# Optimization experiments

Hardware: AMD Instinct MI355X
Metric: run time of the kernel (lower is better)

## Reference

```python
import jax, jax.numpy as jnp
import numpy as np

N_USERS = 150000
N_ENTITIES = 250000
CH = 64
N_REL = 17
N_FACTORS = 4
N_EDGES = 1_000_000
NNZ = 1_000_000
N_HOPS = 2


def setup_inputs() -> dict:
    key = jax.random.key(0)
    ks = jax.random.split(key, 10)
    user_emb = jax.random.normal(ks[0], (N_USERS, CH), jnp.float32) * 0.1
    entity_emb = jax.random.normal(ks[1], (N_ENTITIES, CH), jnp.float32) * 0.1
    latent_emb = jax.random.normal(ks[2], (N_FACTORS, CH), jnp.float32) * 0.1
    weight = jax.random.normal(ks[3], (N_REL - 1, CH), jnp.float32) * 0.1
    disen_weight_att = jax.random.normal(ks[4], (N_FACTORS, N_REL - 1), jnp.float32) * 0.1
    edge_index = jax.random.randint(ks[5], (2, N_EDGES), 0, N_ENTITIES)
    edge_type = jax.random.randint(ks[6], (N_EDGES,), 1, N_REL)  # in [1, N_REL-1]
    inter_row = jax.random.randint(ks[7], (NNZ,), 0, N_USERS)
    inter_col = jax.random.randint(ks[8], (NNZ,), 0, N_ENTITIES)
    inter_val = jax.random.uniform(ks[9], (NNZ,), jnp.float32)
    return {
        "user_emb": user_emb, "entity_emb": entity_emb, "latent_emb": latent_emb,
        "weight": weight, "disen_weight_att": disen_weight_att, "inter_val": inter_val,
        "edge_index": edge_index, "edge_type": edge_type,
        "inter_row": inter_row, "inter_col": inter_col,
    }


def _l2norm(x):
    # F.normalize(x, dim=1) with eps=1e-12
    n = jnp.linalg.norm(x, axis=1, keepdims=True)
    return x / jnp.maximum(n, 1e-12)


def reference(user_emb, entity_emb, latent_emb, weight, disen_weight_att,
              inter_val, edge_index, edge_type, inter_row, inter_col):
    n_entities = entity_emb.shape[0]
    n_users = user_emb.shape[0]
    head, tail = edge_index[0], edge_index[1]

    # _cul_cor with ind='cosine': sum_{i<j} cos(w_i, w_j)^2 over rows of disen_weight_att
    wn = disen_weight_att / jnp.linalg.norm(disen_weight_att, axis=1, keepdims=True)
    gram = (wn @ wn.T) ** 2  # [F, F]
    cor = jnp.sum(jnp.triu(gram, k=1))

    # constants across hops
    counts = jax.ops.segment_sum(jnp.ones(head.shape[0], jnp.float32), head,
                                 num_segments=n_entities)
    denom = jnp.maximum(counts, 1.0)[:, None]  # scatter_mean denominator (0 -> keep 0)
    disen_weight = jax.nn.softmax(disen_weight_att, axis=-1) @ weight  # [F, C]

    e, u = entity_emb, user_emb
    ent_res, usr_res = entity_emb, user_emb
    for _ in range(N_HOPS):
        # KG aggregate: per-edge gather, relation modulation, scatter_mean into heads
        neigh = e[tail] * weight[edge_type - 1]              # [E, C]
        entity_agg = jax.ops.segment_sum(neigh, head, num_segments=n_entities) / denom

        # user -> latent factor attention
        score = jax.nn.softmax(u @ latent_emb.T, axis=1)[:, :, None]  # [U, F, 1]

        # user aggregate: sparse interact_mat @ entity_emb
        user_agg = jax.ops.segment_sum(inter_val[:, None] * e[inter_col], inter_row,
                                       num_segments=n_users)  # [U, C]
        mix = jnp.sum(disen_weight[None, :, :] * score, axis=1)  # [U, C]
        user_agg = user_agg * mix + user_agg

        e = _l2norm(entity_agg)
        u = _l2norm(user_agg)
        ent_res = ent_res + e
        usr_res = usr_res + u
    return ent_res, usr_res, cor
```

## Files before the change

### kernel.cpp

```cpp
#include <hip/hip_runtime.h>
#include <hip/hip_bf16.h>

#define N_USERS    150000
#define N_ENTITIES 250000
#define CHN        64
#define N_RELM1    16
#define N_FACTORS  4
#define N_EDGES    1000000
#define NNZ_       1000000
#define NRECS      (N_EDGES + NNZ_)

#define BROWS      1024
#define RCAP       8192
#define RCAP_OUT   8192
#define EBUCKETS   245
#define USR0       (EBUCKETS * BROWS)
#define ROWS_EFF   (USR0 + N_USERS)
#define NB         392
#define TILE_A     4096
#define TA_THREADS 512
#define ITEMS_A    8
#define BIN_BLOCKS 489
#define CONV_N4    (N_ENTITIES * CHN / 4)
#define CONV_BLOCKS ((CONV_N4 + 511) / 512)

typedef float vf4 __attribute__((ext_vector_type(4)));

__device__ __forceinline__ unsigned short f2bf(float f) {
    unsigned u = __float_as_uint(f);
    return (unsigned short)((u + 0x7fffu + ((u >> 16) & 1u)) >> 16);
}

__global__ __launch_bounds__(512) void build_kernel(
    const int* __restrict__ head, const int* __restrict__ tail,
    const int* __restrict__ etype, const int* __restrict__ irow,
    const int* __restrict__ icol, const float* __restrict__ val,
    int* __restrict__ bcur, unsigned long long* __restrict__ binned,
    const float* __restrict__ weight, const float* __restrict__ att,
    float* __restrict__ disenw, float* __restrict__ cor_out,
    const float4* __restrict__ esrc, ushort4* __restrict__ ebf0)
{
    int blk = blockIdx.x;
    int tid = threadIdx.x;

    if (blk < BIN_BLOCKS) {
        __shared__ int cntS[NB], startS[NB], gbase[NB];
        __shared__ unsigned long long buf[TILE_A];
        __shared__ unsigned short bk[TILE_A];

        if (tid < NB) cntS[tid] = 0;
        __syncthreads();

        int base = blk * TILE_A;
        unsigned long long p[ITEMS_A];
        int bkt[ITEMS_A], rnk[ITEMS_A];
        #pragma unroll
        for (int j = 0; j < ITEMS_A; ++j) {
            int i = base + j * TA_THREADS + tid;
            bkt[j] = -1;
            if (i < NRECS) {
                int row; unsigned long long pay;
                if (i < N_EDGES) {
                    row = head[i];
                    pay = ((unsigned long long)(unsigned)(etype[i] - 1) << 18) | (unsigned)tail[i];
                } else {
                    int jj = i - N_EDGES;
                    row = USR0 + irow[jj];
                    pay = ((unsigned long long)__float_as_uint(val[jj]) << 18) | (unsigned)icol[jj];
                }
                p[j] = pay | ((unsigned long long)(unsigned)(row & (BROWS - 1)) << 50);
                bkt[j] = row >> 10;
                rnk[j] = atomicAdd(&cntS[bkt[j]], 1);
            }
        }
        __syncthreads();
        if (tid == 0) {
            int s = 0;
            for (int b = 0; b < NB; ++b) { startS[b] = s; s += cntS[b]; }
        }
        __syncthreads();
        if (tid < NB && cntS[tid] > 0)
            gbase[tid] = tid * RCAP + atomicAdd(&bcur[tid], cntS[tid]);
        __syncthreads();

        #pragma unroll
        for (int j = 0; j < ITEMS_A; ++j) {
            if (bkt[j] >= 0) {
                int s = startS[bkt[j]] + rnk[j];
                buf[s] = p[j];
                bk[s] = (unsigned short)bkt[j];
            }
        }
        __syncthreads();

        int total = startS[NB - 1] + cntS[NB - 1];
        for (int s = tid; s < total; s += TA_THREADS) {
            int b = bk[s];
            int dst = gbase[b] + (s - startS[b]);
            if (dst < (b + 1) * RCAP) binned[dst] = buf[s];
        }
    } else if (blk == BIN_BLOCKS) {
        if (tid < 256) {
            int f  = tid >> 6;
            int ch = tid & 63;
            float m = -1e30f;
            for (int r = 0; r < N_RELM1; ++r) m = fmaxf(m, att[f * N_RELM1 + r]);
            float ex[N_RELM1];
            float s = 0.f;
            for (int r = 0; r < N_RELM1; ++r) { ex[r] = expf(att[f * N_RELM1 + r] - m); s += ex[r]; }
            float inv = 1.f / s;
            float acc = 0.f;
            for (int r = 0; r < N_RELM1; ++r) acc += (ex[r] * inv) * weight[r * CHN + ch];
            disenw[f * CHN + ch] = acc;
        }
        if (tid == 0) {
            float wn[N_FACTORS][N_RELM1];
            for (int i = 0; i < N_FACTORS; ++i) {
                float ss = 0.f;
                for (int r = 0; r < N_RELM1; ++r) { float v = att[i * N_RELM1 + r]; ss += v * v; }
                float innv = 1.f / sqrtf(ss);
                for (int r = 0; r < N_RELM1; ++r) wn[i][r] = att[i * N_RELM1 + r] * innv;
            }
            float cor = 0.f;
            for (int i = 0; i < N_FACTORS; ++i)
                for (int j = i + 1; j < N_FACTORS; ++j) {
                    float d = 0.f;
                    for (int r = 0; r < N_RELM1; ++r) d += wn[i][r] * wn[j][r];
                    cor += d * d;
                }
            cor_out[0] = cor;
        }
    } else {
        int i = (blk - BIN_BLOCKS - 1) * 512 + tid;
        if (i < CONV_N4) {
            float4 v = esrc[i];
            ebf0[i] = make_ushort4(f2bf(v.x), f2bf(v.y), f2bf(v.z), f2bf(v.w));
        }
    }
}

__global__ __launch_bounds__(512) void bucket_scatter_kernel(
    const unsigned long long* __restrict__ binned,
    const int* __restrict__ bcur,
    unsigned int* __restrict__ recsE,
    unsigned long long* __restrict__ recsU,
    uint4* __restrict__ headerE,
    uint4* __restrict__ headerU)
{
    __shared__ int rowcnt[BROWS];
    __shared__ int sExcl[BROWS];
    __shared__ int sA[512], sB[512];
    __shared__ unsigned int hdr0[BROWS], hdr1[BROWS], hdr2[BROWS];

    int tid = threadIdx.x;
    int b = blockIdx.x;
    rowcnt[2 * tid] = 0;
    rowcnt[2 * tid + 1] = 0;
    hdr0[2 * tid] = 0; hdr0[2 * tid + 1] = 0;
    hdr1[2 * tid] = 0; hdr1[2 * tid + 1] = 0;
    hdr2[2 * tid] = 0; hdr2[2 * tid + 1] = 0;
    __syncthreads();

    int s0 = b * RCAP;
    int nrec = bcur[b];
    if (nrec > RCAP) nrec = RCAP;
    int s1 = s0 + nrec;

    for (int i = s0 + tid; i < s1; i += 512) {
        int rowlo = (int)(binned[i] >> 50) & (BROWS - 1);
        atomicAdd(&rowcnt[rowlo], 1);
    }
    __syncthreads();

    int c0 = rowcnt[2 * tid];
    int c1 = rowcnt[2 * tid + 1];
    int pc0 = (c0 + 1) & ~1;
    int pc1 = (c1 + 1) & ~1;
    sA[tid] = pc0 + pc1;
    __syncthreads();
    int* src = sA; int* dst = sB;
    #pragma unroll
    for (int off = 1; off < 512; off <<= 1) {
        dst[tid] = src[tid] + ((tid >= off) ? src[tid - off] : 0);
        __syncthreads();
        int* tm = src; src = dst; dst = tm;
    }
    int excl = src[tid] - (pc0 + pc1);

    int gbaseOut = (b < EBUCKETS ? b : b - EBUCKETS) * RCAP_OUT;
    __syncthreads();
    rowcnt[2 * tid] = excl;
    rowcnt[2 * tid + 1] = excl + pc0;
    sExcl[2 * tid] = excl;
    sExcl[2 * tid + 1] = excl + pc0;
    __syncthreads();

    if (b < EBUCKETS) {
        for (int i = s0 + tid; i < s1; i += 512) {
            unsigned long long p = binned[i];
            int rowlo = (int)(p >> 50) & (BROWS - 1);
            int local = atomicAdd(&rowcnt[rowlo], 1);
            unsigned rec = (unsigned)(p & ((1ull << 50) - 1));
            recsE[gbaseOut + local] = rec;
            int rank = local - sExcl[rowlo];
            if (rank == 0) hdr0[rowlo] = rec;
            else if (rank == 1) hdr1[rowlo] = rec;
            else if (rank == 2) hdr2[rowlo] = rec;
        }
        __syncthreads();
        int grow = b * BROWS;
        #pragma unroll
        for (int t = 0; t < 2; ++t) {
            int r = 2 * tid + t;
            int row = grow + r;
            if (row < N_ENTITIES) {
                unsigned co = ((unsigned)((t == 0) ? c0 : c1) << 22) |
                              (unsigned)(gbaseOut + sExcl[r]);
                headerE[row] = make_uint4(co, hdr0[r], hdr1[r], hdr2[r]);
            }
        }
    } else {
        for (int i = s0 + tid; i < s1; i += 512) {
            unsigned long long p = binned[i];
            int rowlo = (int)(p >> 50) & (BROWS - 1);
            int local = atomicAdd(&rowcnt[rowlo], 1);
            unsigned long long rec = p & ((1ull << 50) - 1);
            recsU[gbaseOut + local] = rec;
            int rank = local - sExcl[rowlo];
            if (rank == 0) { hdr0[rowlo] = (unsigned)rec; hdr1[rowlo] = (unsigned)(rec >> 32); }
        }
        __syncthreads();
        int grow = b * BROWS - USR0;
        #pragma unroll
        for (int t = 0; t < 2; ++t) {
            int r = 2 * tid + t;
            int urow = grow + r;
            if (urow >= 0 && urow < N_USERS) {
                unsigned co = ((unsigned)((t == 0) ? c0 : c1) << 22) |
                              (unsigned)(gbaseOut + sExcl[r]);
                headerU[urow] = make_uint4(co, hdr0[r], hdr1[r], 0u);
            }
        }
    }
}

__device__ __forceinline__ void fma8w(uint4 g, const float* __restrict__ w, float* acc) {
    acc[0] += __uint_as_float(g.x << 16)          * w[0];
    acc[1] += __uint_as_float(g.x & 0xffff0000u)  * w[1];
    acc[2] += __uint_as_float(g.y << 16)          * w[2];
    acc[3] += __uint_as_float(g.y & 0xffff0000u)  * w[3];
    acc[4] += __uint_as_float(g.z << 16)          * w[4];
    acc[5] += __uint_as_float(g.z & 0xffff0000u)  * w[5];
    acc[6] += __uint_as_float(g.w << 16)          * w[6];
    acc[7] += __uint_as_float(g.w & 0xffff0000u)  * w[7];
}
__device__ __forceinline__ void fma8v(uint4 g, float v, float* acc) {
    acc[0] += __uint_as_float(g.x << 16)          * v;
    acc[1] += __uint_as_float(g.x & 0xffff0000u)  * v;
    acc[2] += __uint_as_float(g.y << 16)          * v;
    acc[3] += __uint_as_float(g.y & 0xffff0000u)  * v;
    acc[4] += __uint_as_float(g.z << 16)          * v;
    acc[5] += __uint_as_float(g.z & 0xffff0000u)  * v;
    acc[6] += __uint_as_float(g.w << 16)          * v;
    acc[7] += __uint_as_float(g.w & 0xffff0000u)  * v;
}
__device__ __forceinline__ void bf8_unpack(uint4 g, float* o) {
    o[0] = __uint_as_float(g.x << 16); o[1] = __uint_as_float(g.x & 0xffff0000u);
    o[2] = __uint_as_float(g.y << 16); o[3] = __uint_as_float(g.y & 0xffff0000u);
    o[4] = __uint_as_float(g.z << 16); o[5] = __uint_as_float(g.z & 0xffff0000u);
    o[6] = __uint_as_float(g.w << 16); o[7] = __uint_as_float(g.w & 0xffff0000u);
}

template<int PASS>
__global__ __launch_bounds__(256) void hop_kernel(
    const unsigned short* __restrict__ ebf,
    const unsigned int* __restrict__ recsE,
    const unsigned long long* __restrict__ recsU,
    const uint4* __restrict__ headerE,
    const uint4* __restrict__ headerU,
    const float* __restrict__ weight,
    const float* __restrict__ latent,
    const float* __restrict__ disenw,
    const float* __restrict__ u_emb,
    const float* __restrict__ e_emb,
    const unsigned short* __restrict__ ubfA,
    unsigned short* __restrict__ ebf_new,
    unsigned short* __restrict__ ubf_new,
    float* __restrict__ out_ent,
    float* __restrict__ out_usr)
{
    __shared__ float wl[N_RELM1 * CHN];
    for (int k = threadIdx.x; k < N_RELM1 * CHN; k += 256) wl[k] = weight[k];
    __syncthreads();

    unsigned idx = blockIdx.x * 256u + threadIdx.x;
    unsigned row = idx >> 3;
    int sub = idx & 7;
    int chb = sub * 8;

    float acc[8] = {0.f,0.f,0.f,0.f,0.f,0.f,0.f,0.f};

    if (row < N_ENTITIES) {
        uint4 h = headerE[row];
        int n = h.x >> 22;
        int start = h.x & 0x3FFFFF;
        if (n > 0) {
            uint4 g = *(const uint4*)(ebf + (size_t)(h.y & 0x3FFFF) * CHN + chb);
            fma8w(g, &wl[(h.y >> 18) * CHN + chb], acc);
        }
        if (n > 1) {
            uint4 g = *(const uint4*)(ebf + (size_t)(h.z & 0x3FFFF) * CHN + chb);
            fma8w(g, &wl[(h.z >> 18) * CHN + chb], acc);
        }
        if (n > 2) {
            uint4 g = *(const uint4*)(ebf + (size_t)(h.w & 0x3FFFF) * CHN + chb);
            fma8w(g, &wl[(h.w >> 18) * CHN + chb], acc);
        }
        int k = 3;
        for (; k + 4 <= n; k += 4) {
            unsigned r0 = recsE[start + k];
            unsigned r1 = recsE[start + k + 1];
            unsigned r2 = recsE[start + k + 2];
            unsigned r3 = recsE[start + k + 3];
            uint4 g0 = *(const uint4*)(ebf + (size_t)(r0 & 0x3FFFF) * CHN + chb);
            uint4 g1 = *(const uint4*)(ebf + (size_t)(r1 & 0x3FFFF) * CHN + chb);
            uint4 g2 = *(const uint4*)(ebf + (size_t)(r2 & 0x3FFFF) * CHN + chb);
            uint4 g3 = *(const uint4*)(ebf + (size_t)(r3 & 0x3FFFF) * CHN + chb);
            fma8w(g0, &wl[(r0 >> 18) * CHN + chb], acc);
            fma8w(g1, &wl[(r1 >> 18) * CHN + chb], acc);
            fma8w(g2, &wl[(r2 >> 18) * CHN + chb], acc);
            fma8w(g3, &wl[(r3 >> 18) * CHN + chb], acc);
        }
        for (; k < n; ++k) {
            unsigned r0 = recsE[start + k];
            uint4 g0 = *(const uint4*)(ebf + (size_t)(r0 & 0x3FFFF) * CHN + chb);
            fma8w(g0, &wl[(r0 >> 18) * CHN + chb], acc);
        }
        float inv_d = (n > 0) ? (1.f / (float)n) : 1.f;
        float ss = 0.f;
        #pragma unroll
        for (int i = 0; i < 8; ++i) { acc[i] *= inv_d; ss += acc[i] * acc[i]; }
        ss += __shfl_xor(ss, 1, 64);
        ss += __shfl_xor(ss, 2, 64);
        ss += __shfl_xor(ss, 4, 64);
        float innv = 1.f / fmaxf(sqrtf(ss), 1e-12f);
        float y[8];
        #pragma unroll
        for (int i = 0; i < 8; ++i) y[i] = acc[i] * innv;
        if (PASS == 1) {
            uint4 pk;
            pk.x = (unsigned)f2bf(y[0]) | ((unsigned)f2bf(y[1]) << 16);
            pk.y = (unsigned)f2bf(y[2]) | ((unsigned)f2bf(y[3]) << 16);
            pk.z = (unsigned)f2bf(y[4]) | ((unsigned)f2bf(y[5]) << 16);
            pk.w = (unsigned)f2bf(y[6]) | ((unsigned)f2bf(y[7]) << 16);
            *(uint4*)(ebf_new + (size_t)row * CHN + chb) = pk;
        } else {
            float y1[8];
            bf8_unpack(*(const uint4*)(ebf + (size_t)row * CHN + chb), y1);
            const vf4* bp = (const vf4*)&e_emb[(size_t)row * CHN + chb];
            vf4 b0 = __builtin_nontemporal_load(bp);
            vf4 b1 = __builtin_nontemporal_load(bp + 1);
            vf4* op = (vf4*)&out_ent[(size_t)row * CHN + chb];
            vf4 o0 = {b0.x + y1[0] + y[0], b0.y + y1[1] + y[1], b0.z + y1[2] + y[2], b0.w + y1[3] + y[3]};
            vf4 o1 = {b1.x + y1[4] + y[4], b1.y + y1[5] + y[5], b1.z + y1[6] + y[6], b1.w + y1[7] + y[7]};
            __builtin_nontemporal_store(o0, op);
            __builtin_nontemporal_store(o1, op + 1);
        }
    } else if (row >= USR0 && row < ROWS_EFF) {
        unsigned ur = row - USR0;
        uint4 h = headerU[ur];
        int n = h.x >> 22;
        int start = h.x & 0x3FFFFF;

        if (n > 0) {
            unsigned long long q = ((unsigned long long)h.z << 32) | h.y;
            uint4 g = *(const uint4*)(ebf + (size_t)(q & 0x3FFFFu) * CHN + chb);
            fma8v(g, __uint_as_float((unsigned)(q >> 18)), acc);
        }
        int k = 1;
        for (; k + 4 <= n; k += 4) {
            unsigned long long q0 = recsU[start + k];
            unsigned long long q1 = recsU[start + k + 1];
            unsigned long long q2 = recsU[start + k + 2];
            unsigned long long q3 = recsU[start + k + 3];
            uint4 g0 = *(const uint4*)(ebf + (size_t)(q0 & 0x3FFFFu) * CHN + chb);
            uint4 g1 = *(const uint4*)(ebf + (size_t)(q1 & 0x3FFFFu) * CHN + chb);
            uint4 g2 = *(const uint4*)(ebf + (size_t)(q2 & 0x3FFFFu) * CHN + chb);
            uint4 g3 = *(const uint4*)(ebf + (size_t)(q3 & 0x3FFFFu) * CHN + chb);
            fma8v(g0, __uint_as_float((unsigned)(q0 >> 18)), acc);
            fma8v(g1, __uint_as_float((unsigned)(q1 >> 18)), acc);
            fma8v(g2, __uint_as_float((unsigned)(q2 >> 18)), acc);
            fma8v(g3, __uint_as_float((unsigned)(q3 >> 18)), acc);
        }
        for (; k < n; ++k) {
            unsigned long long q0 = recsU[start + k];
            uint4 g0 = *(const uint4*)(ebf + (size_t)(q0 & 0x3FFFFu) * CHN + chb);
            fma8v(g0, __uint_as_float((unsigned)(q0 >> 18)), acc);
        }

        float uo[8];
        if (PASS == 1) {
            const float4* up = (const float4*)&u_emb[(size_t)ur * CHN + chb];
            float4 a0 = up[0], a1 = up[1];
            uo[0]=a0.x; uo[1]=a0.y; uo[2]=a0.z; uo[3]=a0.w;
            uo[4]=a1.x; uo[5]=a1.y; uo[6]=a1.z; uo[7]=a1.w;
        } else {
            bf8_unpack(*(const uint4*)(ubfA + (size_t)ur * CHN + chb), uo);
        }

        float dotv[N_FACTORS];
        #pragma unroll
        for (int f = 0; f < N_FACTORS; ++f) {
            const float4* lp = (const float4*)&latent[f * CHN + chb];
            float4 l0 = lp[0], l1 = lp[1];
            float p = uo[0] * l0.x + uo[1] * l0.y + uo[2] * l0.z + uo[3] * l0.w
                    + uo[4] * l1.x + uo[5] * l1.y + uo[6] * l1.z + uo[7] * l1.w;
            p += __shfl_xor(p, 1, 64);
            p += __shfl_xor(p, 2, 64);
            p += __shfl_xor(p, 4, 64);
            dotv[f] = p;
        }
        float m = fmaxf(fmaxf(dotv[0], dotv[1]), fmaxf(dotv[2], dotv[3]));
        float es = 0.f;
        #pragma unroll
        for (int f = 0; f < N_FACTORS; ++f) { dotv[f] = expf(dotv[f] - m); es += dotv[f]; }
        float sinv = 1.f / es;
        float mix[8] = {0.f,0.f,0.f,0.f,0.f,0.f,0.f,0.f};
        #pragma unroll
        for (int f = 0; f < N_FACTORS; ++f) {
            float sc = dotv[f] * sinv;
            const float4* dp = (const float4*)&disenw[f * CHN + chb];
            float4 d0 = dp[0], d1 = dp[1];
            mix[0] += sc * d0.x; mix[1] += sc * d0.y; mix[2] += sc * d0.z; mix[3] += sc * d0.w;
            mix[4] += sc * d1.x; mix[5] += sc * d1.y; mix[6] += sc * d1.z; mix[7] += sc * d1.w;
        }

        float ss = 0.f;
        #pragma unroll
        for (int i = 0; i < 8; ++i) { acc[i] *= (1.f + mix[i]); ss += acc[i] * acc[i]; }
        ss += __shfl_xor(ss, 1, 64);
        ss += __shfl_xor(ss, 2, 64);
        ss += __shfl_xor(ss, 4, 64);
        float innv = 1.f / fmaxf(sqrtf(ss), 1e-12f);
        float y[8];
        #pragma unroll
        for (int i = 0; i < 8; ++i) y[i] = acc[i] * innv;
        if (PASS == 1) {
            uint4 pk;
            pk.x = (unsigned)f2bf(y[0]) | ((unsigned)f2bf(y[1]) << 16);
            pk.y = (unsigned)f2bf(y[2]) | ((unsigned)f2bf(y[3]) << 16);
            pk.z = (unsigned)f2bf(y[4]) | ((unsigned)f2bf(y[5]) << 16);
            pk.w = (unsigned)f2bf(y[6]) | ((unsigned)f2bf(y[7]) << 16);
            *(uint4*)(ubf_new + (size_t)ur * CHN + chb) = pk;
        } else {
            const vf4* bp = (const vf4*)&u_emb[(size_t)ur * CHN + chb];
            vf4 b0 = __builtin_nontemporal_load(bp);
            vf4 b1 = __builtin_nontemporal_load(bp + 1);
            vf4* op = (vf4*)&out_usr[(size_t)ur * CHN + chb];
            vf4 o0 = {b0.x + uo[0] + y[0], b0.y + uo[1] + y[1], b0.z + uo[2] + y[2], b0.w + uo[3] + y[3]};
            vf4 o1 = {b1.x + uo[4] + y[4], b1.y + uo[5] + y[5], b1.z + uo[6] + y[6], b1.w + uo[7] + y[7]};
            __builtin_nontemporal_store(o0, op);
            __builtin_nontemporal_store(o1, op + 1);
        }
    }
}

extern "C" void kernel_launch(void* const* d_in, const int* in_sizes, int n_in,
                              void* d_out, int out_size, void* d_ws, size_t ws_size,
                              hipStream_t stream) {
    const float* user_emb   = (const float*)d_in[0];
    const float* entity_emb = (const float*)d_in[1];
    const float* latent_emb = (const float*)d_in[2];
    const float* weight     = (const float*)d_in[3];
    const float* att        = (const float*)d_in[4];
    const float* inter_val  = (const float*)d_in[5];
    const int*   edge_index = (const int*)d_in[6];
    const int*   edge_type  = (const int*)d_in[7];
    const int*   inter_row  = (const int*)d_in[8];
    const int*   inter_col  = (const int*)d_in[9];

    const int* head = edge_index;
    const int* tail = edge_index + N_EDGES;

    float* out_ent = (float*)d_out;
    float* out_usr = out_ent + (size_t)N_ENTITIES * CHN;
    float* out_cor = out_usr + (size_t)N_USERS * CHN;

    char* ws = (char*)d_ws;
    unsigned short* ebf0   = (unsigned short*)ws;
    unsigned short* ebfA   = (unsigned short*)(ws + 32000000);
    unsigned short* ubfA   = (unsigned short*)(ws + 64000000);
    unsigned long long* binned = (unsigned long long*)(ws + 83200000);
    unsigned long long* recsU  = (unsigned long long*)(ws + 108890112);
    unsigned int* recsE    = (unsigned int*)(ws + 118523904);
    float* disenw          = (float*)(ws + 126552064);
    uint4* headerE         = (uint4*)(ws + 126553088);
    uint4* headerU         = (uint4*)(ws + 130553088);
    int*   bcur            = (int*)(ws + 132953088);

    hipMemsetAsync(bcur, 0, NB * sizeof(int), stream);

    build_kernel<<<BIN_BLOCKS + 1 + CONV_BLOCKS, 512, 0, stream>>>(
        head, tail, edge_type, inter_row, inter_col, inter_val,
        bcur, binned, weight, att, disenw, out_cor,
        (const float4*)entity_emb, (ushort4*)ebf0);

    bucket_scatter_kernel<<<NB, 512, 0, stream>>>(binned, bcur, recsE, recsU,
                                                  headerE, headerU);

    const int hop_blocks = (ROWS_EFF * 8 + 255) / 256;

    hop_kernel<1><<<hop_blocks, 256, 0, stream>>>(ebf0, recsE, recsU, headerE, headerU,
                                                  weight, latent_emb, disenw,
                                                  user_emb, entity_emb, nullptr,
                                                  ebfA, ubfA, nullptr, nullptr);

    hop_kernel<2><<<hop_blocks, 256, 0, stream>>>(ebfA, recsE, recsU, headerE, headerU,
                                                  weight, latent_emb, disenw,
                                                  user_emb, entity_emb, ubfA,
                                                  nullptr, nullptr, out_ent, out_usr);
}
```

Measured before the change: 223.5 us.

## Sort rows by degree within buckets to balance hop kernel wavefronts

The bucket scatter kernel now builds a per-bucket permutation of rows grouped by their edge count (capped at 63) using a shared-memory histogram. The hop kernels read this permutation so that rows of similar degree land in the same wavefront, which cuts divergence from uneven per-row loop lengths. In exchange, every hop thread does one extra indirect load and row writes lose their sequential order within a bucket. Slots for padding rows are marked invalid and skipped.

Measured after the change: 235.4 us. 1.05x slower.

```diff
diff --git a/kernel.cpp b/kernel.cpp
--- a/kernel.cpp
+++ b/kernel.cpp
@@ -17,6 +17,7 @@
 #define USR0       (EBUCKETS * BROWS)
 #define ROWS_EFF   (USR0 + N_USERS)
 #define NB         392
+#define NSLOTS     (NB * BROWS)
 #define TILE_A     4096
 #define TA_THREADS 512
 #define ITEMS_A    8
@@ -145,12 +146,14 @@
     unsigned int* __restrict__ recsE,
     unsigned long long* __restrict__ recsU,
     uint4* __restrict__ headerE,
-    uint4* __restrict__ headerU)
+    uint4* __restrict__ headerU,
+    unsigned int* __restrict__ perm)
 {
     __shared__ int rowcnt[BROWS];
     __shared__ int sExcl[BROWS];
     __shared__ int sA[512], sB[512];
     __shared__ unsigned int hdr0[BROWS], hdr1[BROWS], hdr2[BROWS];
+    __shared__ int dh[64], dhoff[64];
 
     int tid = threadIdx.x;
     int b = blockIdx.x;
@@ -159,6 +162,7 @@
     hdr0[2 * tid] = 0; hdr0[2 * tid + 1] = 0;
     hdr1[2 * tid] = 0; hdr1[2 * tid + 1] = 0;
     hdr2[2 * tid] = 0; hdr2[2 * tid + 1] = 0;
+    if (tid < 64) dh[tid] = 0;
     __syncthreads();
 
     int s0 = b * RCAP;
@@ -193,6 +197,24 @@
     rowcnt[2 * tid + 1] = excl + pc0;
     sExcl[2 * tid] = excl;
     sExcl[2 * tid + 1] = excl + pc0;
+
+    int grow = b * BROWS;
+    bool v0, v1;
+    if (b < EBUCKETS) { v0 = (grow + 2 * tid) < N_ENTITIES; v1 = (grow + 2 * tid + 1) < N_ENTITIES; }
+    else              { v0 = (grow + 2 * tid) < ROWS_EFF;   v1 = (grow + 2 * tid + 1) < ROWS_EFF; }
+    int key0 = v0 ? min(c0, 63) : 0;
+    int key1 = v1 ? min(c1, 63) : 0;
+    int rank0 = atomicAdd(&dh[key0], 1);
+    int rank1 = atomicAdd(&dh[key1], 1);
+    __syncthreads();
+    if (tid == 0) {
+        int s = 0;
+        #pragma unroll
+        for (int i = 0; i < 64; ++i) { dhoff[i] = s; s += dh[i]; }
+    }
+    __syncthreads();
+    perm[grow + dhoff[key0] + rank0] = v0 ? (unsigned)(grow + 2 * tid)     : 0xFFFFFFFFu;
+    perm[grow + dhoff[key1] + rank1] = v1 ? (unsigned)(grow + 2 * tid + 1) : 0xFFFFFFFFu;
     __syncthreads();
 
     if (b < EBUCKETS) {
@@ -208,7 +230,6 @@
             else if (rank == 2) hdr2[rowlo] = rec;
         }
         __syncthreads();
-        int grow = b * BROWS;
         #pragma unroll
         for (int t = 0; t < 2; ++t) {
             int r = 2 * tid + t;
@@ -230,11 +251,11 @@
             if (rank == 0) { hdr0[rowlo] = (unsigned)rec; hdr1[rowlo] = (unsigned)(rec >> 32); }
         }
         __syncthreads();
-        int grow = b * BROWS - USR0;
+        int ubase = grow - USR0;
         #pragma unroll
         for (int t = 0; t < 2; ++t) {
             int r = 2 * tid + t;
-            int urow = grow + r;
+            int urow = ubase + r;
             if (urow >= 0 && urow < N_USERS) {
                 unsigned co = ((unsigned)((t == 0) ? c0 : c1) << 22) |
                               (unsigned)(gbaseOut + sExcl[r]);
@@ -278,6 +299,7 @@
     const unsigned long long* __restrict__ recsU,
     const uint4* __restrict__ headerE,
     const uint4* __restrict__ headerU,
+    const unsigned int* __restrict__ perm,
     const float* __restrict__ weight,
     const float* __restrict__ latent,
     const float* __restrict__ disenw,
@@ -294,9 +316,11 @@
     __syncthreads();
 
     unsigned idx = blockIdx.x * 256u + threadIdx.x;
-    unsigned row = idx >> 3;
+    unsigned slot = idx >> 3;
     int sub = idx & 7;
     int chb = sub * 8;
+    if (slot >= NSLOTS) return;
+    unsigned row = perm[slot];
 
     float acc[8] = {0.f,0.f,0.f,0.f,0.f,0.f,0.f,0.f};
 
@@ -366,7 +390,7 @@
             __builtin_nontemporal_store(o0, op);
             __builtin_nontemporal_store(o1, op + 1);
         }
-    } else if (row >= USR0 && row < ROWS_EFF) {
+    } else if (row < ROWS_EFF) {
         unsigned ur = row - USR0;
         uint4 h = headerU[ur];
         int n = h.x >> 22;
@@ -496,7 +520,8 @@
     float* disenw          = (float*)(ws + 126552064);
     uint4* headerE         = (uint4*)(ws + 126553088);
     uint4* headerU         = (uint4*)(ws + 130553088);
-    int*   bcur            = (int*)(ws + 132953088);
+    unsigned int* perm     = (unsigned int*)(ws + 132953088);
+    int*   bcur            = (int*)(ws + 134558720);
 
     hipMemsetAsync(bcur, 0, NB * sizeof(int), stream);
 
@@ -506,16 +531,16 @@
         (const float4*)entity_emb, (ushort4*)ebf0);
 
     bucket_scatter_kernel<<<NB, 512, 0, stream>>>(binned, bcur, recsE, recsU,
-                                                  headerE, headerU);
-
-    const int hop_blocks = (ROWS_EFF * 8 + 255) / 256;
-
-    hop_kernel<1><<<hop_blocks, 256, 0, stream>>>(ebf0, recsE, recsU, headerE, headerU,
+                                                  headerE, headerU, perm);
+
+    const int hop_blocks = (NSLOTS * 8) / 256;
+
+    hop_kernel<1><<<hop_blocks, 256, 0, stream>>>(ebf0, recsE, recsU, headerE, headerU, perm,
                                                   weight, latent_emb, disenw,
                                                   user_emb, entity_emb, nullptr,
                                                   ebfA, ubfA, nullptr, nullptr);
 
-    hop_kernel<2><<<hop_blocks, 256, 0, stream>>>(ebfA, recsE, recsU, headerE, headerU,
+    hop_kernel<2><<<hop_blocks, 256, 0, stream>>>(ebfA, recsE, recsU, headerE, headerU, perm,
                                                   weight, latent_emb, disenw,
                                                   user_emb, entity_emb, ubfA,
                                                   nullptr, nullptr, out_ent, out_usr);
```
